# Optimization experiments

Measured on AMD Instinct MI355X. Metric: run time of the kernel, lower is better.

## Reference

```python
import jax, jax.numpy as jnp
import numpy as np

M_MARGIN = 0.5
SCALE = 64.0
COS_M = float(np.cos(M_MARGIN))
SIN_M = float(np.sin(M_MARGIN))
TH = -COS_M
MM = SIN_M * M_MARGIN
NUM_CLASSES = 100000
IN_FEATURES = 512
BATCH = 512


def setup_inputs() -> dict:
    key = jax.random.key(0)
    k1, k2, k3 = jax.random.split(key, 3)
    x = jax.random.normal(k1, (BATCH, IN_FEATURES), dtype=jnp.float32)
    y = jax.random.randint(k2, (BATCH,), 0, NUM_CLASSES, dtype=jnp.int64 if jax.config.jax_enable_x64 else jnp.int32)
    # xavier_uniform-like init for weight [num_classes, in_features]
    limit = float(np.sqrt(6.0 / (NUM_CLASSES + IN_FEATURES)))
    weight = jax.random.uniform(k3, (NUM_CLASSES, IN_FEATURES), minval=-limit, maxval=limit, dtype=jnp.float32)
    return {"x": x, "y": y, "weight": weight}


def _l2_normalize(v, axis=-1, eps=1e-12):
    # matches F.normalize(p=2): v / max(||v||, eps)
    n = jnp.sqrt(jnp.sum(v * v, axis=axis, keepdims=True))
    return v / jnp.maximum(n, eps)


def reference(x, y, weight):
    # cosine logits: [B, C]
    xn = _l2_normalize(x)
    wn = _l2_normalize(weight)
    cos = jnp.einsum('bd,cd->bc', xn, wn)
    sin = jnp.sqrt(jnp.clip(1.0 - cos * cos, 0.0))
    cos_w_margin = cos * COS_M - sin * SIN_M
    cos_w_margin = jnp.where(cos > TH, cos_w_margin, cos - MM)
    ohe = jax.nn.one_hot(y, NUM_CLASSES, dtype=jnp.bool_)
    logit = jnp.where(ohe, cos_w_margin, cos) * SCALE
    # cross entropy, mean reduction
    logp = jax.nn.log_softmax(logit, axis=-1)
    nll = -jnp.take_along_axis(logp, y[:, None], axis=-1)[:, 0]
    return jnp.mean(nll)
```

## Files before the change

### kernel.cpp

```cpp
#include <hip/hip_runtime.h>
#include <hip/hip_bf16.h>
#include <cstdint>
#include <cstddef>

#define C_CLS   100000
#define D_FEAT  512
#define B_ROWS  512

#define COSM 0.8775825618903728f
#define SINM 0.479425538604203f
#define TH_  (-0.8775825618903728f)
#define MM_  0.2397127693021015f

typedef __bf16 bf16x8 __attribute__((ext_vector_type(8)));
typedef __bf16 bf16x4 __attribute__((ext_vector_type(4)));
typedef float  f32x4  __attribute__((ext_vector_type(4)));

typedef __attribute__((address_space(3))) void lds_void;
typedef const __attribute__((address_space(1))) void g_void;

__device__ __forceinline__ void async_copy16(const void* g, void* l) {
    __builtin_amdgcn_global_load_lds((g_void*)g, (lds_void*)l, 16, 0, 0);
}

__global__ void k_xnorm(const float* __restrict__ x, __bf16* __restrict__ xn,
                        float* __restrict__ row_sum, float* __restrict__ tlogit) {
    const int row  = blockIdx.x;
    const int lane = threadIdx.x;
    const f32x4* p = (const f32x4*)(x + (size_t)row * D_FEAT);
    f32x4 a = p[lane];
    f32x4 b = p[lane + 64];
    float s = a[0]*a[0] + a[1]*a[1] + a[2]*a[2] + a[3]*a[3]
            + b[0]*b[0] + b[1]*b[1] + b[2]*b[2] + b[3]*b[3];
    #pragma unroll
    for (int m = 32; m >= 1; m >>= 1) s += __shfl_xor(s, m, 64);
    const float inv = 1.0f / fmaxf(sqrtf(s), 1e-12f);
    bf16x4 o0 = { (__bf16)(a[0]*inv), (__bf16)(a[1]*inv), (__bf16)(a[2]*inv), (__bf16)(a[3]*inv) };
    bf16x4 o1 = { (__bf16)(b[0]*inv), (__bf16)(b[1]*inv), (__bf16)(b[2]*inv), (__bf16)(b[3]*inv) };
    *(bf16x4*)(xn + (size_t)row * D_FEAT + lane * 4)       = o0;
    *(bf16x4*)(xn + (size_t)row * D_FEAT + 256 + lane * 4) = o1;
    if (lane == 0) { row_sum[row] = 0.0f; tlogit[row] = 0.0f; }
}

__global__ void k_wnorm(const float* __restrict__ w, float* __restrict__ inv_wn) {
    const int row  = blockIdx.x * 4 + (threadIdx.x >> 6);
    const int lane = threadIdx.x & 63;
    if (row >= C_CLS) return;
    const f32x4* p = (const f32x4*)(w + (size_t)row * D_FEAT);
    f32x4 a = p[lane];
    f32x4 b = p[lane + 64];
    float s = a[0]*a[0] + a[1]*a[1] + a[2]*a[2] + a[3]*a[3]
            + b[0]*b[0] + b[1]*b[1] + b[2]*b[2] + b[3]*b[3];
    #pragma unroll
    for (int m = 32; m >= 1; m >>= 1) s += __shfl_xor(s, m, 64);
    if (lane == 0) inv_wn[row] = 1.0f / fmaxf(sqrtf(s), 1e-12f);
}

__global__ __launch_bounds__(256, 2) void k_gemm(
        const __bf16* __restrict__ xn, const float* __restrict__ w,
        const float* __restrict__ inv_wn, const int* __restrict__ y,
        float* __restrict__ row_sum, float* __restrict__ tlogit) {

    __shared__ __align__(16) __bf16 As[4 * 128 * 8];
    __shared__ __align__(16) float  Bs[4 * 128 * 8];
    __shared__ int ys[128];

    const int tid = threadIdx.x;
    const int bm  = blockIdx.x & 3;
    const int bn  = blockIdx.x >> 2;

    if (tid < 128) ys[tid] = y[bm * 128 + tid];

    const int wave = tid >> 6;
    const int lane = tid & 63;
    const int wm   = wave >> 1;
    const int wn   = wave & 1;
    const int quad = lane >> 4;
    const int l15  = lane & 15;

    f32x4 acc[4][4];
    #pragma unroll
    for (int i = 0; i < 4; ++i)
        #pragma unroll
        for (int j = 0; j < 4; ++j) acc[i][j] = (f32x4){0.f, 0.f, 0.f, 0.f};

    for (int kt = 0; kt < 16; ++kt) {
        const int k0 = kt * 32;
        #pragma unroll
        for (int i = 0; i < 2; ++i) {
            const int c  = tid + i * 256;
            const int qc = c >> 7, rc = c & 127;
            const __bf16* g = xn + (size_t)(bm * 128 + rc) * D_FEAT + k0 + qc * 8;
            async_copy16(g, &As[(size_t)c * 8]);
        }
        #pragma unroll
        for (int i = 0; i < 4; ++i) {
            const int c  = tid + i * 256;
            const int qc = c >> 8, rc = (c >> 1) & 127, hc = c & 1;
            int grow = bn * 128 + rc; if (grow > C_CLS - 1) grow = C_CLS - 1;
            const float* g = w + (size_t)grow * D_FEAT + k0 + qc * 8 + hc * 4;
            async_copy16(g, &Bs[(size_t)c * 4]);
        }
        __syncthreads();

        bf16x8 af[4];
        #pragma unroll
        for (int mi = 0; mi < 4; ++mi) {
            const int r = wm * 64 + mi * 16 + l15;
            af[mi] = *(const bf16x8*)&As[(size_t)(quad * 128 + r) * 8];
        }
        bf16x8 bfr[4];
        #pragma unroll
        for (int ni = 0; ni < 4; ++ni) {
            const int r = wn * 64 + ni * 16 + l15;
            const float* bp = &Bs[(size_t)(quad * 128 + r) * 8];
            f32x4 b0 = *(const f32x4*)bp;
            f32x4 b1 = *(const f32x4*)(bp + 4);
            bf16x8 t;
            t[0] = (__bf16)b0[0]; t[1] = (__bf16)b0[1]; t[2] = (__bf16)b0[2]; t[3] = (__bf16)b0[3];
            t[4] = (__bf16)b1[0]; t[5] = (__bf16)b1[1]; t[6] = (__bf16)b1[2]; t[7] = (__bf16)b1[3];
            bfr[ni] = t;
        }
        #pragma unroll
        for (int mi = 0; mi < 4; ++mi)
            #pragma unroll
            for (int ni = 0; ni < 4; ++ni)
                acc[mi][ni] = __builtin_amdgcn_mfma_f32_16x16x32_bf16(af[mi], bfr[ni], acc[mi][ni], 0, 0, 0);
        __syncthreads();
    }

    #pragma unroll
    for (int mi = 0; mi < 4; ++mi) {
        float rs[4] = {0.f, 0.f, 0.f, 0.f};
        #pragma unroll
        for (int ni = 0; ni < 4; ++ni) {
            const int lcol = wn * 64 + ni * 16 + l15;
            const int gcol = bn * 128 + lcol;
            const bool colv = (gcol < C_CLS);
            const float invw = inv_wn[colv ? gcol : (C_CLS - 1)];
            #pragma unroll
            for (int reg = 0; reg < 4; ++reg) {
                const int lrow = wm * 64 + mi * 16 + quad * 4 + reg;
                const float cosv = acc[mi][ni][reg] * invw;
                const float sinv = sqrtf(fmaxf(1.0f - cosv * cosv, 0.0f));
                const float phi  = (cosv > TH_) ? (cosv * COSM - sinv * SINM) : (cosv - MM_);
                const bool ist   = colv && (gcol == ys[lrow]);
                const float logit = 64.0f * (ist ? phi : cosv);
                if (ist) tlogit[bm * 128 + lrow] = logit;
                rs[reg] += colv ? __expf(logit - 64.0f) : 0.0f;
            }
        }
        #pragma unroll
        for (int reg = 0; reg < 4; ++reg) {
            float v = rs[reg];
            v += __shfl_xor(v, 8, 64);
            v += __shfl_xor(v, 4, 64);
            v += __shfl_xor(v, 2, 64);
            v += __shfl_xor(v, 1, 64);
            if (l15 == 0) {
                const int lrow = wm * 64 + mi * 16 + quad * 4 + reg;
                atomicAdd(&row_sum[bm * 128 + lrow], v);
            }
        }
    }
}

__global__ void k_final(const float* __restrict__ row_sum, const float* __restrict__ tlogit,
                        float* __restrict__ out) {
    const int t = threadIdx.x;
    float v = logf(row_sum[t]) + 64.0f - tlogit[t];
    #pragma unroll
    for (int m = 32; m >= 1; m >>= 1) v += __shfl_xor(v, m, 64);
    __shared__ float partial[8];
    if ((t & 63) == 0) partial[t >> 6] = v;
    __syncthreads();
    if (t == 0) {
        float s = 0.f;
        #pragma unroll
        for (int i = 0; i < 8; ++i) s += partial[i];
        out[0] = s * (1.0f / 512.0f);
    }
}

extern "C" void kernel_launch(void* const* d_in, const int* in_sizes, int n_in,
                              void* d_out, int out_size, void* d_ws, size_t ws_size,
                              hipStream_t stream) {
    const float* x = (const float*)d_in[0];
    const int*   y = (const int*)d_in[1];
    const float* w = (const float*)d_in[2];

    char* ws = (char*)d_ws;
    __bf16* xn      = (__bf16*)ws;
    float*  inv_wn  = (float*)(ws + 524288);
    float*  row_sum = (float*)(ws + 524288 + 400000);
    float*  tlogit  = (float*)(ws + 524288 + 400000 + 2048);
    float*  out     = (float*)d_out;

    hipLaunchKernelGGL(k_xnorm, dim3(512), dim3(64), 0, stream, x, xn, row_sum, tlogit);
    hipLaunchKernelGGL(k_wnorm, dim3(25000), dim3(256), 0, stream, w, inv_wn);
    hipLaunchKernelGGL(k_gemm, dim3(4 * 782), dim3(256), 0, stream, xn, w, inv_wn, y, row_sum, tlogit);
    hipLaunchKernelGGL(k_final, dim3(1), dim3(512), 0, stream, row_sum, tlogit, out);
}
```

Before: 500.0 us.

## Pre-normalize weights to bf16 in norm kernel and stream bf16 into GEMM

The weight-norm kernel now writes a fully normalized bf16 copy of the weight matrix instead of only per-row inverse norms. The GEMM loads that bf16 copy straight into LDS, so the per-tile fp32-to-bf16 conversion, the doubled fp32 B traffic and the per-column inverse-norm scaling in the epilogue all go away. In exchange, an extra ~100MB bf16 intermediate is written and read back through a larger workspace. Total HBM traffic stays roughly the same, but it is moved out of the GEMM's inner loop.

```diff
diff --git a/kernel.cpp b/kernel.cpp
--- a/kernel.cpp
+++ b/kernel.cpp
@@ -42,7 +42,7 @@
     if (lane == 0) { row_sum[row] = 0.0f; tlogit[row] = 0.0f; }
 }
 
-__global__ void k_wnorm(const float* __restrict__ w, float* __restrict__ inv_wn) {
+__global__ void k_wnorm(const float* __restrict__ w, __bf16* __restrict__ wn) {
     const int row  = blockIdx.x * 4 + (threadIdx.x >> 6);
     const int lane = threadIdx.x & 63;
     if (row >= C_CLS) return;
@@ -53,16 +53,20 @@
             + b[0]*b[0] + b[1]*b[1] + b[2]*b[2] + b[3]*b[3];
     #pragma unroll
     for (int m = 32; m >= 1; m >>= 1) s += __shfl_xor(s, m, 64);
-    if (lane == 0) inv_wn[row] = 1.0f / fmaxf(sqrtf(s), 1e-12f);
+    const float inv = 1.0f / fmaxf(sqrtf(s), 1e-12f);
+    bf16x4 o0 = { (__bf16)(a[0]*inv), (__bf16)(a[1]*inv), (__bf16)(a[2]*inv), (__bf16)(a[3]*inv) };
+    bf16x4 o1 = { (__bf16)(b[0]*inv), (__bf16)(b[1]*inv), (__bf16)(b[2]*inv), (__bf16)(b[3]*inv) };
+    *(bf16x4*)(wn + (size_t)row * D_FEAT + lane * 4)       = o0;
+    *(bf16x4*)(wn + (size_t)row * D_FEAT + 256 + lane * 4) = o1;
 }
 
 __global__ __launch_bounds__(256, 2) void k_gemm(
-        const __bf16* __restrict__ xn, const float* __restrict__ w,
-        const float* __restrict__ inv_wn, const int* __restrict__ y,
+        const __bf16* __restrict__ xn, const __bf16* __restrict__ wn,
+        const int* __restrict__ y,
         float* __restrict__ row_sum, float* __restrict__ tlogit) {
 
     __shared__ __align__(16) __bf16 As[4 * 128 * 8];
-    __shared__ __align__(16) float  Bs[4 * 128 * 8];
+    __shared__ __align__(16) __bf16 Bs[4 * 128 * 8];
     __shared__ int ys[128];
 
     const int tid = threadIdx.x;
@@ -74,7 +78,7 @@
     const int wave = tid >> 6;
     const int lane = tid & 63;
     const int wm   = wave >> 1;
-    const int wn   = wave & 1;
+    const int wn_  = wave & 1;
     const int quad = lane >> 4;
     const int l15  = lane & 15;
 
@@ -90,36 +94,29 @@
         for (int i = 0; i < 2; ++i) {
             const int c  = tid + i * 256;
             const int qc = c >> 7, rc = c & 127;
-            const __bf16* g = xn + (size_t)(bm * 128 + rc) * D_FEAT + k0 + qc * 8;
-            async_copy16(g, &As[(size_t)c * 8]);
+            const __bf16* ga = xn + (size_t)(bm * 128 + rc) * D_FEAT + k0 + qc * 8;
+            async_copy16(ga, &As[(size_t)c * 8]);
         }
         #pragma unroll
-        for (int i = 0; i < 4; ++i) {
+        for (int i = 0; i < 2; ++i) {
             const int c  = tid + i * 256;
-            const int qc = c >> 8, rc = (c >> 1) & 127, hc = c & 1;
+            const int qc = c >> 7, rc = c & 127;
             int grow = bn * 128 + rc; if (grow > C_CLS - 1) grow = C_CLS - 1;
-            const float* g = w + (size_t)grow * D_FEAT + k0 + qc * 8 + hc * 4;
-            async_copy16(g, &Bs[(size_t)c * 4]);
+            const __bf16* gb = wn + (size_t)grow * D_FEAT + k0 + qc * 8;
+            async_copy16(gb, &Bs[(size_t)c * 8]);
         }
         __syncthreads();
 
-        bf16x8 af[4];
+        bf16x8 af[4], bfr[4];
         #pragma unroll
         for (int mi = 0; mi < 4; ++mi) {
             const int r = wm * 64 + mi * 16 + l15;
             af[mi] = *(const bf16x8*)&As[(size_t)(quad * 128 + r) * 8];
         }
-        bf16x8 bfr[4];
         #pragma unroll
         for (int ni = 0; ni < 4; ++ni) {
-            const int r = wn * 64 + ni * 16 + l15;
-            const float* bp = &Bs[(size_t)(quad * 128 + r) * 8];
-            f32x4 b0 = *(const f32x4*)bp;
-            f32x4 b1 = *(const f32x4*)(bp + 4);
-            bf16x8 t;
-            t[0] = (__bf16)b0[0]; t[1] = (__bf16)b0[1]; t[2] = (__bf16)b0[2]; t[3] = (__bf16)b0[3];
-            t[4] = (__bf16)b1[0]; t[5] = (__bf16)b1[1]; t[6] = (__bf16)b1[2]; t[7] = (__bf16)b1[3];
-            bfr[ni] = t;
+            const int r = wn_ * 64 + ni * 16 + l15;
+            bfr[ni] = *(const bf16x8*)&Bs[(size_t)(quad * 128 + r) * 8];
         }
         #pragma unroll
         for (int mi = 0; mi < 4; ++mi)
@@ -134,14 +131,13 @@
         float rs[4] = {0.f, 0.f, 0.f, 0.f};
         #pragma unroll
         for (int ni = 0; ni < 4; ++ni) {
-            const int lcol = wn * 64 + ni * 16 + l15;
+            const int lcol = wn_ * 64 + ni * 16 + l15;
             const int gcol = bn * 128 + lcol;
             const bool colv = (gcol < C_CLS);
-            const float invw = inv_wn[colv ? gcol : (C_CLS - 1)];
             #pragma unroll
             for (int reg = 0; reg < 4; ++reg) {
                 const int lrow = wm * 64 + mi * 16 + quad * 4 + reg;
-                const float cosv = acc[mi][ni][reg] * invw;
+                const float cosv = acc[mi][ni][reg];
                 const float sinv = sqrtf(fmaxf(1.0f - cosv * cosv, 0.0f));
                 const float phi  = (cosv > TH_) ? (cosv * COSM - sinv * SINM) : (cosv - MM_);
                 const bool ist   = colv && (gcol == ys[lrow]);
@@ -191,13 +187,13 @@
 
     char* ws = (char*)d_ws;
     __bf16* xn      = (__bf16*)ws;
-    float*  inv_wn  = (float*)(ws + 524288);
-    float*  row_sum = (float*)(ws + 524288 + 400000);
-    float*  tlogit  = (float*)(ws + 524288 + 400000 + 2048);
+    __bf16* wnorm   = (__bf16*)(ws + 524288);
+    float*  row_sum = (float*)(ws + 524288 + 102400000);
+    float*  tlogit  = (float*)(ws + 524288 + 102400000 + 2048);
     float*  out     = (float*)d_out;
 
     hipLaunchKernelGGL(k_xnorm, dim3(512), dim3(64), 0, stream, x, xn, row_sum, tlogit);
-    hipLaunchKernelGGL(k_wnorm, dim3(25000), dim3(256), 0, stream, w, inv_wn);
-    hipLaunchKernelGGL(k_gemm, dim3(4 * 782), dim3(256), 0, stream, xn, w, inv_wn, y, row_sum, tlogit);
+    hipLaunchKernelGGL(k_wnorm, dim3(25000), dim3(256), 0, stream, w, wnorm);
+    hipLaunchKernelGGL(k_gemm, dim3(4 * 782), dim3(256), 0, stream, xn, wnorm, y, row_sum, tlogit);
     hipLaunchKernelGGL(k_final, dim3(1), dim3(512), 0, stream, row_sum, tlogit, out);
 }
```

After: 509.7 us. No clear change (+2.0%).
